# Optimization experiments

Hardware: AMD Instinct MI355X
Metric: run time of the kernel (lower is better)

## Reference

```python
import jax, jax.numpy as jnp
import numpy as np

WH, WW = 7, 7
N_HEADS = 6
INPUT_DIM = 192
HEAD_DIM = INPUT_DIM // N_HEADS
QK_SCALE = HEAD_DIM ** (-0.5)


def _relative_position_index(wh, ww):
    coords = np.stack(np.meshgrid(np.arange(wh), np.arange(ww), indexing='ij'))  # (2, wh, ww)
    cf = coords.reshape(2, -1)                       # (2, N)
    rel = cf[:, :, None] - cf[:, None, :]            # (2, N, N)
    rel = rel.transpose(1, 2, 0).copy()              # (N, N, 2)
    rel[:, :, 0] += wh - 1
    rel[:, :, 1] += ww - 1
    rel[:, :, 0] *= 2 * ww - 1
    return jnp.asarray(rel.sum(-1), dtype=jnp.int32)  # (N, N)

_REL_IDX = _relative_position_index(WH, WW)


def setup_inputs() -> dict:
    key = jax.random.key(0)
    ks = jax.random.split(key, 7)
    bW, nW = 4096, 64
    N = WH * WW
    s = 0.02
    return {
        "x": jax.random.normal(ks[0], (bW, WH, WW, INPUT_DIM), jnp.float32),
        "mask": jax.random.normal(ks[1], (nW, N, N), jnp.float32),
        "qkv_w": jax.random.normal(ks[2], (3 * INPUT_DIM, INPUT_DIM), jnp.float32) * s,
        "qkv_b": jax.random.normal(ks[3], (3 * INPUT_DIM,), jnp.float32) * s,
        "out_w": jax.random.normal(ks[4], (INPUT_DIM, INPUT_DIM), jnp.float32) * s,
        "out_b": jax.random.normal(ks[5], (INPUT_DIM,), jnp.float32) * s,
        "rpb_table": jax.random.normal(ks[6], ((2 * WH - 1) * (2 * WW - 1), N_HEADS), jnp.float32) * s,
    }


def reference(x, mask, qkv_w, qkv_b, out_w, out_b, rpb_table):
    b, Wh, Ww, C = x.shape
    N = Wh * Ww
    H, D = N_HEADS, HEAD_DIM
    # 1x1 conv == pointwise linear over channels-last input
    qkv = jnp.einsum('bxyc,oc->bxyo', x, qkv_w) + qkv_b          # (b, Wh, Ww, 3C)
    qkv = qkv.reshape(b, N, 3, H, D)                             # chunk order q,k,v; (h d) channel layout
    q, k, v = qkv[:, :, 0], qkv[:, :, 1], qkv[:, :, 2]           # (b, N, H, D)
    q = q * QK_SCALE
    sim = jnp.einsum('bihd,bjhd->bhij', q, k)                    # (b, H, N, N)
    # relative position bias gather
    rpb = rpb_table[_REL_IDX]                                    # (N, N, H)
    sim = sim + rpb.transpose(2, 0, 1)[None]                     # + (1, H, N, N)
    # shift mask add over windows
    nW = mask.shape[0]
    sim = sim.reshape(b // nW, nW, H, N, N) + mask[None, :, None]
    attn = jax.nn.softmax(sim, axis=-1).reshape(b, H, N, N)
    out = jnp.einsum('bhij,bjhd->bihd', attn, v)                 # (b, N, H, D)
    out = out.reshape(b, N, H * D)                               # (h d) channel order
    out = jnp.einsum('bnc,oc->bno', out, out_w) + out_b
    return out.reshape(b, Wh, Ww, C)
```

## Files before the change

### kernel.cpp

```cpp
#include <hip/hip_runtime.h>
#include <hip/hip_bf16.h>

typedef __bf16 bf16;
typedef __bf16 bf16x8 __attribute__((ext_vector_type(8)));
typedef float f32x4 __attribute__((ext_vector_type(4)));
typedef float floatv4 __attribute__((ext_vector_type(4)));

#define QK_SCALE 0.17677669529663687f

__device__ __forceinline__ bf16* qk_ptr(bf16* base, int row, int col) {
    return base + row * 32 + ((((col >> 3) ^ ((row >> 1) & 3)) << 3)) + (col & 7);
}
__device__ __forceinline__ bf16* vt_ptr(bf16* base, int row, int col) {
    return base + row * 64 + ((((col >> 3) ^ (row & 7)) << 3)) + (col & 7);
}
__device__ __forceinline__ bf16* ao_ptr(bf16* base, int row, int col) {
    return base + row * 192 + ((((col >> 3) ^ (row & 7)) << 3)) + (col & 7);
}

__global__ void wmsa_prep(const float* __restrict__ qkv_w,
                          const float* __restrict__ out_w,
                          const float* __restrict__ rpb_table,
                          const float* __restrict__ mask,
                          bf16* __restrict__ qkv_wb,
                          bf16* __restrict__ out_wb,
                          float* __restrict__ rpbx,
                          float* __restrict__ combo,
                          int build_combo) {
    int t = blockIdx.x * 256 + threadIdx.x;
    if (t < 110592) qkv_wb[t] = (bf16)qkv_w[t];
    if (t < 36864)  out_wb[t] = (bf16)out_w[t];
    if (t < 14406) {
        int h = t / 2401, ij = t % 2401, i = ij / 49, j = ij % 49;
        int ri = (i / 7 - j / 7 + 6) * 13 + (i % 7 - j % 7 + 6);
        rpbx[t] = rpb_table[ri * 6 + h];
    }
    if (build_combo && t < 64 * 6 * 64 * 64) {
        int j = t & 63, i = (t >> 6) & 63, r = t >> 12;
        int h = r % 6, w = r / 6;
        float v = -1e30f;
        if (i < 49 && j < 49) {
            int ri = (i / 7 - j / 7 + 6) * 13 + (i % 7 - j % 7 + 6);
            v = rpb_table[ri * 6 + h] + mask[w * 2401 + i * 49 + j];
        }
        combo[t] = v;
    }
}

template <bool USE_COMBO>
__global__ __launch_bounds__(768, 3) void wmsa_fused(
    const float* __restrict__ x, const float* __restrict__ mask,
    const float* __restrict__ qkv_b, const float* __restrict__ out_b,
    const bf16* __restrict__ qkv_wb, const bf16* __restrict__ out_wb,
    const float* __restrict__ rpbx, const float* __restrict__ combo,
    float* __restrict__ out)
{
    __shared__ __align__(16) bf16 s_x[12288];
    __shared__ __align__(16) bf16 s_qp[6][2048];
    __shared__ __align__(16) bf16 s_kao[12288];
    __shared__ __align__(16) bf16 s_vt[6][2048];

    const int b    = blockIdx.x;
    const int tid  = threadIdx.x;
    const int wv   = tid >> 6;
    const int lane = tid & 63;
    const int lo   = lane & 15;
    const int hi   = lane >> 4;

    const float* xw    = x + (size_t)b * 9408;
    const int    obase = wv * 48;
    const int    sec   = wv >> 2;

    {
        const int c0 = tid;
        const int r0s = c0 / 24, cc0 = c0 % 24;
        const float* p0 = xw + r0s * 192 + cc0 * 8;
        floatv4 f0 = *(const floatv4*)p0;
        floatv4 f1 = *(const floatv4*)(p0 + 4);
        bf16x8 v;
        v[0]=(bf16)f0[0]; v[1]=(bf16)f0[1]; v[2]=(bf16)f0[2]; v[3]=(bf16)f0[3];
        v[4]=(bf16)f1[0]; v[5]=(bf16)f1[1]; v[6]=(bf16)f1[2]; v[7]=(bf16)f1[3];
        *(bf16x8*)&s_x[(r0s * 24 + (cc0 ^ (r0s & 7))) * 8] = v;

        const int c1 = tid + 768;
        const int r1s = c1 / 24, cc1 = c1 % 24;
        bf16x8 w = {};
        if (r1s < 49) {
            const float* p1 = xw + r1s * 192 + cc1 * 8;
            floatv4 g0 = *(const floatv4*)p1;
            floatv4 g1 = *(const floatv4*)(p1 + 4);
            w[0]=(bf16)g0[0]; w[1]=(bf16)g0[1]; w[2]=(bf16)g0[2]; w[3]=(bf16)g0[3];
            w[4]=(bf16)g1[0]; w[5]=(bf16)g1[1]; w[6]=(bf16)g1[2]; w[7]=(bf16)g1[3];
        }
        *(bf16x8*)&s_x[(r1s * 24 + (cc1 ^ (r1s & 7))) * 8] = w;
    }
    __syncthreads();

#pragma unroll 1
    for (int mib = 0; mib < 2; ++mib) {
        f32x4 acc[2][3];
#pragma unroll
        for (int mi = 0; mi < 2; ++mi)
#pragma unroll
            for (int nj = 0; nj < 3; ++nj) acc[mi][nj] = (f32x4){0.f, 0.f, 0.f, 0.f};

        const int r0 = mib * 32 + lo;
        const int r1 = r0 + 16;

        auto loadB = [&](bf16x8* dst, int kk) {
#pragma unroll
            for (int nj = 0; nj < 3; ++nj)
                dst[nj] = *(const bf16x8*)(qkv_wb + (obase + nj * 16 + lo) * 192 + kk * 32 + hi * 8);
        };

        bf16x8 b0_[3], b1_[3], b2_[3];
        loadB(b0_, 0);
        loadB(b1_, 1);
#pragma unroll
        for (int kk = 0; kk < 6; ++kk) {
            if (kk < 4) loadB(b2_, kk + 2);
            bf16x8 a0 = *(const bf16x8*)ao_ptr(s_x, r0, kk * 32 + hi * 8);
            bf16x8 a1 = *(const bf16x8*)ao_ptr(s_x, r1, kk * 32 + hi * 8);
            acc[0][0] = __builtin_amdgcn_mfma_f32_16x16x32_bf16(a0, b0_[0], acc[0][0], 0, 0, 0);
            acc[1][0] = __builtin_amdgcn_mfma_f32_16x16x32_bf16(a1, b0_[0], acc[1][0], 0, 0, 0);
            acc[0][1] = __builtin_amdgcn_mfma_f32_16x16x32_bf16(a0, b0_[1], acc[0][1], 0, 0, 0);
            acc[1][1] = __builtin_amdgcn_mfma_f32_16x16x32_bf16(a1, b0_[1], acc[1][1], 0, 0, 0);
            acc[0][2] = __builtin_amdgcn_mfma_f32_16x16x32_bf16(a0, b0_[2], acc[0][2], 0, 0, 0);
            acc[1][2] = __builtin_amdgcn_mfma_f32_16x16x32_bf16(a1, b0_[2], acc[1][2], 0, 0, 0);
            b0_[0] = b1_[0]; b0_[1] = b1_[1]; b0_[2] = b1_[2];
            b1_[0] = b2_[0]; b1_[1] = b2_[1]; b1_[2] = b2_[2];
        }

#pragma unroll
        for (int nj = 0; nj < 3; ++nj) {
            const int o    = obase + nj * 16 + lo;
            const float bs = qkv_b[o];
            const int oc   = o - sec * 192;
            const int hh   = oc >> 5;
            const int dd   = oc & 31;
#pragma unroll
            for (int mi = 0; mi < 2; ++mi)
#pragma unroll
                for (int r = 0; r < 4; ++r) {
                    const int n = mib * 32 + mi * 16 + hi * 4 + r;
                    const float v = acc[mi][nj][r] + bs;
                    if (sec == 0)      *qk_ptr(&s_qp[hh][0], n, dd)      = (bf16)(v * QK_SCALE);
                    else if (sec == 1) *qk_ptr(s_kao + hh * 2048, n, dd) = (bf16)v;
                    else               *vt_ptr(&s_vt[hh][0], dd, n)      = (bf16)v;
                }
        }
    }
    __syncthreads();

    {
        const int h    = wv >> 1;
        const int p    = wv & 1;
        const int rowb = p * 32;
        bf16* qb    = &s_qp[h][0];
        bf16* kbase = s_kao + h * 2048;

        f32x4 cv[2][4];
        if (USE_COMBO) {
            const float* cb = combo + (((size_t)(b & 63) * 6 + h) << 12);
#pragma unroll
            for (int mi = 0; mi < 2; ++mi)
#pragma unroll
                for (int nt = 0; nt < 4; ++nt)
#pragma unroll
                    for (int r = 0; r < 4; ++r)
                        cv[mi][nt][r] = cb[(rowb + mi * 16 + hi * 4 + r) * 64 + nt * 16 + lo];
        }

        bf16x8 qa0 = *(const bf16x8*)qk_ptr(qb, rowb + lo, hi * 8);
        bf16x8 qa1 = *(const bf16x8*)qk_ptr(qb, rowb + 16 + lo, hi * 8);
        bf16x8 kb0 = *(const bf16x8*)qk_ptr(kbase,  0 + lo, hi * 8);
        bf16x8 kb1 = *(const bf16x8*)qk_ptr(kbase, 16 + lo, hi * 8);
        bf16x8 kb2 = *(const bf16x8*)qk_ptr(kbase, 32 + lo, hi * 8);
        bf16x8 kb3 = *(const bf16x8*)qk_ptr(kbase, 48 + lo, hi * 8);

        __syncthreads();

        f32x4 s[2][4];
#pragma unroll
        for (int mi = 0; mi < 2; ++mi)
#pragma unroll
            for (int nt = 0; nt < 4; ++nt) s[mi][nt] = (f32x4){0.f, 0.f, 0.f, 0.f};
        s[0][0] = __builtin_amdgcn_mfma_f32_16x16x32_bf16(qa0, kb0, s[0][0], 0, 0, 0);
        s[0][1] = __builtin_amdgcn_mfma_f32_16x16x32_bf16(qa0, kb1, s[0][1], 0, 0, 0);
        s[0][2] = __builtin_amdgcn_mfma_f32_16x16x32_bf16(qa0, kb2, s[0][2], 0, 0, 0);
        s[0][3] = __builtin_amdgcn_mfma_f32_16x16x32_bf16(qa0, kb3, s[0][3], 0, 0, 0);
        s[1][0] = __builtin_amdgcn_mfma_f32_16x16x32_bf16(qa1, kb0, s[1][0], 0, 0, 0);
        s[1][1] = __builtin_amdgcn_mfma_f32_16x16x32_bf16(qa1, kb1, s[1][1], 0, 0, 0);
        s[1][2] = __builtin_amdgcn_mfma_f32_16x16x32_bf16(qa1, kb2, s[1][2], 0, 0, 0);
        s[1][3] = __builtin_amdgcn_mfma_f32_16x16x32_bf16(qa1, kb3, s[1][3], 0, 0, 0);

        if (USE_COMBO) {
#pragma unroll
            for (int mi = 0; mi < 2; ++mi)
#pragma unroll
                for (int nt = 0; nt < 4; ++nt) s[mi][nt] += cv[mi][nt];
        } else {
            const float* mk = mask + (size_t)(b & 63) * 2401;
            const float* rb = rpbx + h * 2401;
#pragma unroll
            for (int nt = 0; nt < 4; ++nt) {
                const int j = nt * 16 + lo;
#pragma unroll
                for (int mi = 0; mi < 2; ++mi)
#pragma unroll
                    for (int r = 0; r < 4; ++r) {
                        const int i = rowb + mi * 16 + hi * 4 + r;
                        float sv = s[mi][nt][r];
                        if (j >= 49 || i >= 49) sv = -1e30f;
                        else sv += rb[i * 49 + j] + mk[i * 49 + j];
                        s[mi][nt][r] = sv;
                    }
            }
        }

#pragma unroll
        for (int mi = 0; mi < 2; ++mi)
#pragma unroll
            for (int r = 0; r < 4; ++r) {
                float m = fmaxf(fmaxf(s[mi][0][r], s[mi][1][r]),
                                fmaxf(s[mi][2][r], s[mi][3][r]));
                m = fmaxf(m, __shfl_xor(m, 1));
                m = fmaxf(m, __shfl_xor(m, 2));
                m = fmaxf(m, __shfl_xor(m, 4));
                m = fmaxf(m, __shfl_xor(m, 8));
                float sum = 0.f;
#pragma unroll
                for (int nt = 0; nt < 4; ++nt) {
                    float pv = __expf(s[mi][nt][r] - m);
                    s[mi][nt][r] = pv;
                    sum += pv;
                }
                sum += __shfl_xor(sum, 1);
                sum += __shfl_xor(sum, 2);
                sum += __shfl_xor(sum, 4);
                sum += __shfl_xor(sum, 8);
                const float inv = 1.0f / sum;
#pragma unroll
                for (int nt = 0; nt < 4; ++nt) s[mi][nt][r] *= inv;
            }

        f32x4 o00 = (f32x4){0.f,0.f,0.f,0.f}, o01 = (f32x4){0.f,0.f,0.f,0.f};
        f32x4 o10 = (f32x4){0.f,0.f,0.f,0.f}, o11 = (f32x4){0.f,0.f,0.f,0.f};
#pragma unroll
        for (int kk = 0; kk < 2; ++kk) {
#pragma unroll
            for (int mi = 0; mi < 2; ++mi)
#pragma unroll
                for (int c = 0; c < 2; ++c) {
                    const int nt = kk * 2 + c;
#pragma unroll
                    for (int r = 0; r < 4; ++r)
                        *qk_ptr(qb, rowb + mi * 16 + hi * 4 + r, c * 16 + lo) =
                            (bf16)s[mi][nt][r];
                }
            bf16x8 pa0 = *(const bf16x8*)qk_ptr(qb, rowb + lo, hi * 8);
            bf16x8 pa1 = *(const bf16x8*)qk_ptr(qb, rowb + 16 + lo, hi * 8);
            bf16x8 vb0 = *(const bf16x8*)vt_ptr(&s_vt[h][0],  0 + lo, kk * 32 + hi * 8);
            bf16x8 vb1 = *(const bf16x8*)vt_ptr(&s_vt[h][0], 16 + lo, kk * 32 + hi * 8);
            o00 = __builtin_amdgcn_mfma_f32_16x16x32_bf16(pa0, vb0, o00, 0, 0, 0);
            o10 = __builtin_amdgcn_mfma_f32_16x16x32_bf16(pa1, vb0, o10, 0, 0, 0);
            o01 = __builtin_amdgcn_mfma_f32_16x16x32_bf16(pa0, vb1, o01, 0, 0, 0);
            o11 = __builtin_amdgcn_mfma_f32_16x16x32_bf16(pa1, vb1, o11, 0, 0, 0);
        }

#pragma unroll
        for (int r = 0; r < 4; ++r) {
            const int n0 = rowb + hi * 4 + r;
            const int n1 = n0 + 16;
            *ao_ptr(s_kao, n0, h * 32 +  0 + lo) = (bf16)o00[r];
            *ao_ptr(s_kao, n0, h * 32 + 16 + lo) = (bf16)o01[r];
            *ao_ptr(s_kao, n1, h * 32 +  0 + lo) = (bf16)o10[r];
            *ao_ptr(s_kao, n1, h * 32 + 16 + lo) = (bf16)o11[r];
        }
    }
    __syncthreads();

    {
        const int o2 = wv * 16 + lo;
        f32x4 facc[4];
#pragma unroll
        for (int mi = 0; mi < 4; ++mi) facc[mi] = (f32x4){0.f, 0.f, 0.f, 0.f};

        bf16x8 fbc = *(const bf16x8*)(out_wb + o2 * 192 + hi * 8);
#pragma unroll
        for (int kk = 0; kk < 6; ++kk) {
            bf16x8 fbn;
            if (kk < 5) fbn = *(const bf16x8*)(out_wb + o2 * 192 + (kk + 1) * 32 + hi * 8);
            bf16x8 fa[4];
#pragma unroll
            for (int mi = 0; mi < 4; ++mi)
                fa[mi] = *(const bf16x8*)ao_ptr(s_kao, mi * 16 + lo, kk * 32 + hi * 8);
#pragma unroll
            for (int mi = 0; mi < 4; ++mi)
                facc[mi] = __builtin_amdgcn_mfma_f32_16x16x32_bf16(fa[mi], fbc, facc[mi], 0, 0, 0);
            fbc = fbn;
        }

        const float ob = out_b[o2];
        float* ow = out + (size_t)b * 9408;
#pragma unroll
        for (int mi = 0; mi < 4; ++mi)
#pragma unroll
            for (int r = 0; r < 4; ++r) {
                const int n = mi * 16 + hi * 4 + r;
                if (n < 49) ow[n * 192 + o2] = facc[mi][r] + ob;
            }
    }
}

extern "C" void kernel_launch(void* const* d_in, const int* in_sizes, int n_in,
                              void* d_out, int out_size, void* d_ws, size_t ws_size,
                              hipStream_t stream) {
    const float* x      = (const float*)d_in[0];
    const float* mask   = (const float*)d_in[1];
    const float* qkv_w  = (const float*)d_in[2];
    const float* qkv_b  = (const float*)d_in[3];
    const float* out_w  = (const float*)d_in[4];
    const float* out_b  = (const float*)d_in[5];
    const float* rpb    = (const float*)d_in[6];
    float* out          = (float*)d_out;

    char* ws = (char*)d_ws;
    bf16*  qkv_wb = (bf16*)ws;
    bf16*  out_wb = (bf16*)(ws + 221184);
    float* rpbx   = (float*)(ws + 294912);
    float* combo  = (float*)(ws + 352768);
    const bool use_combo = ws_size >= (size_t)(352768 + 6291456);

    hipLaunchKernelGGL(wmsa_prep, dim3(6144), dim3(256), 0, stream,
                       qkv_w, out_w, rpb, mask, qkv_wb, out_wb, rpbx, combo,
                       use_combo ? 1 : 0);
    if (use_combo)
        hipLaunchKernelGGL(HIP_KERNEL_NAME(wmsa_fused<true>), dim3(4096), dim3(768), 0, stream,
                           x, mask, qkv_b, out_b, qkv_wb, out_wb, rpbx, combo, out);
    else
        hipLaunchKernelGGL(HIP_KERNEL_NAME(wmsa_fused<false>), dim3(4096), dim3(768), 0, stream,
                           x, mask, qkv_b, out_b, qkv_wb, out_wb, rpbx, combo, out);
}
```

Measured before the change: 309.0 us.

## Transpose attention scores layout, vectorize LDS stores, prefetch combo bias and out weights

Computes S^T = K·Q^T so each lane holds a full query row's column slices, which reduces the softmax reductions to two cross-row shuffles. Q/K and V projections are written to LDS as packed 4-element bf16 stores using swapped MFMA operands. The combo bias table is stored transposed and loaded at kernel start, and all out-projection weights are loaded before the final barrier, so global latency overlaps earlier phases. The cost is higher register pressure at 768 threads with a minimum of 3 blocks per SM, which risks spills.

```diff
diff --git a/kernel.cpp b/kernel.cpp
--- a/kernel.cpp
+++ b/kernel.cpp
@@ -2,6 +2,7 @@
 #include <hip/hip_bf16.h>
 
 typedef __bf16 bf16;
+typedef __bf16 bf16x4 __attribute__((ext_vector_type(4)));
 typedef __bf16 bf16x8 __attribute__((ext_vector_type(8)));
 typedef float f32x4 __attribute__((ext_vector_type(4)));
 typedef float floatv4 __attribute__((ext_vector_type(4)));
@@ -25,7 +26,7 @@
                           bf16* __restrict__ qkv_wb,
                           bf16* __restrict__ out_wb,
                           float* __restrict__ rpbx,
-                          float* __restrict__ combo,
+                          float* __restrict__ comboT,
                           int build_combo) {
     int t = blockIdx.x * 256 + threadIdx.x;
     if (t < 110592) qkv_wb[t] = (bf16)qkv_w[t];
@@ -36,14 +37,14 @@
         rpbx[t] = rpb_table[ri * 6 + h];
     }
     if (build_combo && t < 64 * 6 * 64 * 64) {
-        int j = t & 63, i = (t >> 6) & 63, r = t >> 12;
+        int i = t & 63, j = (t >> 6) & 63, r = t >> 12;
         int h = r % 6, w = r / 6;
         float v = -1e30f;
         if (i < 49 && j < 49) {
             int ri = (i / 7 - j / 7 + 6) * 13 + (i % 7 - j % 7 + 6);
             v = rpb_table[ri * 6 + h] + mask[w * 2401 + i * 49 + j];
         }
-        combo[t] = v;
+        comboT[t] = v;
     }
 }
 
@@ -52,7 +53,7 @@
     const float* __restrict__ x, const float* __restrict__ mask,
     const float* __restrict__ qkv_b, const float* __restrict__ out_b,
     const bf16* __restrict__ qkv_wb, const bf16* __restrict__ out_wb,
-    const float* __restrict__ rpbx, const float* __restrict__ combo,
+    const float* __restrict__ rpbx, const float* __restrict__ comboT,
     float* __restrict__ out)
 {
     __shared__ __align__(16) bf16 s_x[12288];
@@ -70,6 +71,22 @@
     const float* xw    = x + (size_t)b * 9408;
     const int    obase = wv * 48;
     const int    sec   = wv >> 2;
+
+    const int ah   = wv >> 1;
+    const int arow = (wv & 1) * 32;
+
+    f32x4 cvT[2][4];
+    if (USE_COMBO) {
+        const float* cbT = comboT + (((size_t)(b & 63) * 6 + ah) << 12);
+#pragma unroll
+        for (int mq = 0; mq < 2; ++mq)
+#pragma unroll
+            for (int nt = 0; nt < 4; ++nt)
+#pragma unroll
+                for (int r = 0; r < 4; ++r)
+                    cvT[mq][nt][r] =
+                        cbT[(nt * 16 + hi * 4 + r) * 64 + arow + mq * 16 + lo];
+    }
 
     {
         const int c0 = tid;
@@ -121,163 +138,189 @@
             if (kk < 4) loadB(b2_, kk + 2);
             bf16x8 a0 = *(const bf16x8*)ao_ptr(s_x, r0, kk * 32 + hi * 8);
             bf16x8 a1 = *(const bf16x8*)ao_ptr(s_x, r1, kk * 32 + hi * 8);
-            acc[0][0] = __builtin_amdgcn_mfma_f32_16x16x32_bf16(a0, b0_[0], acc[0][0], 0, 0, 0);
-            acc[1][0] = __builtin_amdgcn_mfma_f32_16x16x32_bf16(a1, b0_[0], acc[1][0], 0, 0, 0);
-            acc[0][1] = __builtin_amdgcn_mfma_f32_16x16x32_bf16(a0, b0_[1], acc[0][1], 0, 0, 0);
-            acc[1][1] = __builtin_amdgcn_mfma_f32_16x16x32_bf16(a1, b0_[1], acc[1][1], 0, 0, 0);
-            acc[0][2] = __builtin_amdgcn_mfma_f32_16x16x32_bf16(a0, b0_[2], acc[0][2], 0, 0, 0);
-            acc[1][2] = __builtin_amdgcn_mfma_f32_16x16x32_bf16(a1, b0_[2], acc[1][2], 0, 0, 0);
+            if (sec < 2) {
+#pragma unroll
+                for (int nj = 0; nj < 3; ++nj) {
+                    acc[0][nj] = __builtin_amdgcn_mfma_f32_16x16x32_bf16(b0_[nj], a0, acc[0][nj], 0, 0, 0);
+                    acc[1][nj] = __builtin_amdgcn_mfma_f32_16x16x32_bf16(b0_[nj], a1, acc[1][nj], 0, 0, 0);
+                }
+            } else {
+#pragma unroll
+                for (int nj = 0; nj < 3; ++nj) {
+                    acc[0][nj] = __builtin_amdgcn_mfma_f32_16x16x32_bf16(a0, b0_[nj], acc[0][nj], 0, 0, 0);
+                    acc[1][nj] = __builtin_amdgcn_mfma_f32_16x16x32_bf16(a1, b0_[nj], acc[1][nj], 0, 0, 0);
+                }
+            }
             b0_[0] = b1_[0]; b0_[1] = b1_[1]; b0_[2] = b1_[2];
             b1_[0] = b2_[0]; b1_[1] = b2_[1]; b1_[2] = b2_[2];
         }
 
-#pragma unroll
-        for (int nj = 0; nj < 3; ++nj) {
-            const int o    = obase + nj * 16 + lo;
-            const float bs = qkv_b[o];
-            const int oc   = o - sec * 192;
-            const int hh   = oc >> 5;
-            const int dd   = oc & 31;
-#pragma unroll
-            for (int mi = 0; mi < 2; ++mi)
-#pragma unroll
-                for (int r = 0; r < 4; ++r) {
-                    const int n = mib * 32 + mi * 16 + hi * 4 + r;
-                    const float v = acc[mi][nj][r] + bs;
-                    if (sec == 0)      *qk_ptr(&s_qp[hh][0], n, dd)      = (bf16)(v * QK_SCALE);
-                    else if (sec == 1) *qk_ptr(s_kao + hh * 2048, n, dd) = (bf16)v;
-                    else               *vt_ptr(&s_vt[hh][0], dd, n)      = (bf16)v;
-                }
+        if (sec < 2) {
+#pragma unroll
+            for (int nj = 0; nj < 3; ++nj) {
+                const int ob4 = obase + nj * 16 + hi * 4;
+                floatv4 bs4 = *(const floatv4*)(qkv_b + ob4);
+                const int oc0 = ob4 - sec * 192;
+                const int hh  = oc0 >> 5;
+                const int dd  = oc0 & 31;
+                bf16* base = (sec == 0) ? &s_qp[hh][0] : (s_kao + hh * 2048);
+#pragma unroll
+                for (int mi = 0; mi < 2; ++mi) {
+                    const int n = mib * 32 + mi * 16 + lo;
+                    bf16x4 pk;
+#pragma unroll
+                    for (int r = 0; r < 4; ++r) {
+                        float v = acc[mi][nj][r] + bs4[r];
+                        if (sec == 0) v *= QK_SCALE;
+                        pk[r] = (bf16)v;
+                    }
+                    *(bf16x4*)qk_ptr(base, n, dd) = pk;
+                }
+            }
+        } else {
+#pragma unroll
+            for (int nj = 0; nj < 3; ++nj) {
+                const int o  = obase + nj * 16 + lo;
+                const float bs = qkv_b[o];
+                const int oc = o - 384;
+                const int hh = oc >> 5;
+                const int dd = oc & 31;
+#pragma unroll
+                for (int mi = 0; mi < 2; ++mi) {
+                    const int n0 = mib * 32 + mi * 16 + hi * 4;
+                    bf16x4 pk;
+#pragma unroll
+                    for (int r = 0; r < 4; ++r)
+                        pk[r] = (bf16)(acc[mi][nj][r] + bs);
+                    *(bf16x4*)vt_ptr(&s_vt[hh][0], dd, n0) = pk;
+                }
+            }
         }
     }
     __syncthreads();
 
+    f32x4 oacc[2][2];
+    bf16x8 fb[6];
     {
-        const int h    = wv >> 1;
-        const int p    = wv & 1;
-        const int rowb = p * 32;
-        bf16* qb    = &s_qp[h][0];
-        bf16* kbase = s_kao + h * 2048;
-
-        f32x4 cv[2][4];
+        bf16* qb    = &s_qp[ah][0];
+        bf16* kbase = s_kao + ah * 2048;
+
+        bf16x8 ka0 = *(const bf16x8*)qk_ptr(kbase,  0 + lo, hi * 8);
+        bf16x8 ka1 = *(const bf16x8*)qk_ptr(kbase, 16 + lo, hi * 8);
+        bf16x8 ka2 = *(const bf16x8*)qk_ptr(kbase, 32 + lo, hi * 8);
+        bf16x8 ka3 = *(const bf16x8*)qk_ptr(kbase, 48 + lo, hi * 8);
+        bf16x8 qb0 = *(const bf16x8*)qk_ptr(qb, arow + lo, hi * 8);
+        bf16x8 qb1 = *(const bf16x8*)qk_ptr(qb, arow + 16 + lo, hi * 8);
+
+        f32x4 t[4][2];
+#pragma unroll
+        for (int nt = 0; nt < 4; ++nt)
+#pragma unroll
+            for (int mq = 0; mq < 2; ++mq) t[nt][mq] = (f32x4){0.f, 0.f, 0.f, 0.f};
+        t[0][0] = __builtin_amdgcn_mfma_f32_16x16x32_bf16(ka0, qb0, t[0][0], 0, 0, 0);
+        t[1][0] = __builtin_amdgcn_mfma_f32_16x16x32_bf16(ka1, qb0, t[1][0], 0, 0, 0);
+        t[2][0] = __builtin_amdgcn_mfma_f32_16x16x32_bf16(ka2, qb0, t[2][0], 0, 0, 0);
+        t[3][0] = __builtin_amdgcn_mfma_f32_16x16x32_bf16(ka3, qb0, t[3][0], 0, 0, 0);
+        t[0][1] = __builtin_amdgcn_mfma_f32_16x16x32_bf16(ka0, qb1, t[0][1], 0, 0, 0);
+        t[1][1] = __builtin_amdgcn_mfma_f32_16x16x32_bf16(ka1, qb1, t[1][1], 0, 0, 0);
+        t[2][1] = __builtin_amdgcn_mfma_f32_16x16x32_bf16(ka2, qb1, t[2][1], 0, 0, 0);
+        t[3][1] = __builtin_amdgcn_mfma_f32_16x16x32_bf16(ka3, qb1, t[3][1], 0, 0, 0);
+
         if (USE_COMBO) {
-            const float* cb = combo + (((size_t)(b & 63) * 6 + h) << 12);
-#pragma unroll
-            for (int mi = 0; mi < 2; ++mi)
-#pragma unroll
-                for (int nt = 0; nt < 4; ++nt)
-#pragma unroll
-                    for (int r = 0; r < 4; ++r)
-                        cv[mi][nt][r] = cb[(rowb + mi * 16 + hi * 4 + r) * 64 + nt * 16 + lo];
-        }
-
-        bf16x8 qa0 = *(const bf16x8*)qk_ptr(qb, rowb + lo, hi * 8);
-        bf16x8 qa1 = *(const bf16x8*)qk_ptr(qb, rowb + 16 + lo, hi * 8);
-        bf16x8 kb0 = *(const bf16x8*)qk_ptr(kbase,  0 + lo, hi * 8);
-        bf16x8 kb1 = *(const bf16x8*)qk_ptr(kbase, 16 + lo, hi * 8);
-        bf16x8 kb2 = *(const bf16x8*)qk_ptr(kbase, 32 + lo, hi * 8);
-        bf16x8 kb3 = *(const bf16x8*)qk_ptr(kbase, 48 + lo, hi * 8);
-
-        __syncthreads();
-
-        f32x4 s[2][4];
-#pragma unroll
-        for (int mi = 0; mi < 2; ++mi)
-#pragma unroll
-            for (int nt = 0; nt < 4; ++nt) s[mi][nt] = (f32x4){0.f, 0.f, 0.f, 0.f};
-        s[0][0] = __builtin_amdgcn_mfma_f32_16x16x32_bf16(qa0, kb0, s[0][0], 0, 0, 0);
-        s[0][1] = __builtin_amdgcn_mfma_f32_16x16x32_bf16(qa0, kb1, s[0][1], 0, 0, 0);
-        s[0][2] = __builtin_amdgcn_mfma_f32_16x16x32_bf16(qa0, kb2, s[0][2], 0, 0, 0);
-        s[0][3] = __builtin_amdgcn_mfma_f32_16x16x32_bf16(qa0, kb3, s[0][3], 0, 0, 0);
-        s[1][0] = __builtin_amdgcn_mfma_f32_16x16x32_bf16(qa1, kb0, s[1][0], 0, 0, 0);
-        s[1][1] = __builtin_amdgcn_mfma_f32_16x16x32_bf16(qa1, kb1, s[1][1], 0, 0, 0);
-        s[1][2] = __builtin_amdgcn_mfma_f32_16x16x32_bf16(qa1, kb2, s[1][2], 0, 0, 0);
-        s[1][3] = __builtin_amdgcn_mfma_f32_16x16x32_bf16(qa1, kb3, s[1][3], 0, 0, 0);
-
-        if (USE_COMBO) {
-#pragma unroll
-            for (int mi = 0; mi < 2; ++mi)
-#pragma unroll
-                for (int nt = 0; nt < 4; ++nt) s[mi][nt] += cv[mi][nt];
+#pragma unroll
+            for (int nt = 0; nt < 4; ++nt)
+#pragma unroll
+                for (int mq = 0; mq < 2; ++mq) t[nt][mq] += cvT[mq][nt];
         } else {
             const float* mk = mask + (size_t)(b & 63) * 2401;
-            const float* rb = rpbx + h * 2401;
-#pragma unroll
-            for (int nt = 0; nt < 4; ++nt) {
-                const int j = nt * 16 + lo;
-#pragma unroll
-                for (int mi = 0; mi < 2; ++mi)
+            const float* rb = rpbx + ah * 2401;
+#pragma unroll
+            for (int nt = 0; nt < 4; ++nt)
+#pragma unroll
+                for (int mq = 0; mq < 2; ++mq)
 #pragma unroll
                     for (int r = 0; r < 4; ++r) {
-                        const int i = rowb + mi * 16 + hi * 4 + r;
-                        float sv = s[mi][nt][r];
+                        const int i = arow + mq * 16 + lo;
+                        const int j = nt * 16 + hi * 4 + r;
+                        float sv = t[nt][mq][r];
                         if (j >= 49 || i >= 49) sv = -1e30f;
                         else sv += rb[i * 49 + j] + mk[i * 49 + j];
-                        s[mi][nt][r] = sv;
+                        t[nt][mq][r] = sv;
                     }
-            }
-        }
-
-#pragma unroll
-        for (int mi = 0; mi < 2; ++mi)
-#pragma unroll
-            for (int r = 0; r < 4; ++r) {
-                float m = fmaxf(fmaxf(s[mi][0][r], s[mi][1][r]),
-                                fmaxf(s[mi][2][r], s[mi][3][r]));
-                m = fmaxf(m, __shfl_xor(m, 1));
-                m = fmaxf(m, __shfl_xor(m, 2));
-                m = fmaxf(m, __shfl_xor(m, 4));
-                m = fmaxf(m, __shfl_xor(m, 8));
-                float sum = 0.f;
-#pragma unroll
-                for (int nt = 0; nt < 4; ++nt) {
-                    float pv = __expf(s[mi][nt][r] - m);
-                    s[mi][nt][r] = pv;
-                    sum += pv;
-                }
-                sum += __shfl_xor(sum, 1);
-                sum += __shfl_xor(sum, 2);
-                sum += __shfl_xor(sum, 4);
-                sum += __shfl_xor(sum, 8);
-                const float inv = 1.0f / sum;
-#pragma unroll
-                for (int nt = 0; nt < 4; ++nt) s[mi][nt][r] *= inv;
-            }
-
-        f32x4 o00 = (f32x4){0.f,0.f,0.f,0.f}, o01 = (f32x4){0.f,0.f,0.f,0.f};
-        f32x4 o10 = (f32x4){0.f,0.f,0.f,0.f}, o11 = (f32x4){0.f,0.f,0.f,0.f};
+        }
+
+#pragma unroll
+        for (int mq = 0; mq < 2; ++mq) {
+            float m = fmaxf(fmaxf(t[0][mq][0], t[0][mq][1]),
+                            fmaxf(t[0][mq][2], t[0][mq][3]));
+#pragma unroll
+            for (int nt = 1; nt < 4; ++nt)
+                m = fmaxf(m, fmaxf(fmaxf(t[nt][mq][0], t[nt][mq][1]),
+                                   fmaxf(t[nt][mq][2], t[nt][mq][3])));
+            m = fmaxf(m, __shfl_xor(m, 16));
+            m = fmaxf(m, __shfl_xor(m, 32));
+            float sum = 0.f;
+#pragma unroll
+            for (int nt = 0; nt < 4; ++nt)
+#pragma unroll
+                for (int r = 0; r < 4; ++r) {
+                    float e = __expf(t[nt][mq][r] - m);
+                    t[nt][mq][r] = e;
+                    sum += e;
+                }
+            sum += __shfl_xor(sum, 16);
+            sum += __shfl_xor(sum, 32);
+            const float inv = 1.0f / sum;
+#pragma unroll
+            for (int nt = 0; nt < 4; ++nt)
+#pragma unroll
+                for (int r = 0; r < 4; ++r) t[nt][mq][r] *= inv;
+        }
+
+        {
+            const int o2 = wv * 16 + lo;
+#pragma unroll
+            for (int kk = 0; kk < 6; ++kk)
+                fb[kk] = *(const bf16x8*)(out_wb + o2 * 192 + kk * 32 + hi * 8);
+        }
+
+#pragma unroll
+        for (int mq = 0; mq < 2; ++mq)
+#pragma unroll
+            for (int nd = 0; nd < 2; ++nd) oacc[mq][nd] = (f32x4){0.f, 0.f, 0.f, 0.f};
+
 #pragma unroll
         for (int kk = 0; kk < 2; ++kk) {
 #pragma unroll
-            for (int mi = 0; mi < 2; ++mi)
+            for (int mq = 0; mq < 2; ++mq)
 #pragma unroll
                 for (int c = 0; c < 2; ++c) {
                     const int nt = kk * 2 + c;
-#pragma unroll
-                    for (int r = 0; r < 4; ++r)
-                        *qk_ptr(qb, rowb + mi * 16 + hi * 4 + r, c * 16 + lo) =
-                            (bf16)s[mi][nt][r];
-                }
-            bf16x8 pa0 = *(const bf16x8*)qk_ptr(qb, rowb + lo, hi * 8);
-            bf16x8 pa1 = *(const bf16x8*)qk_ptr(qb, rowb + 16 + lo, hi * 8);
-            bf16x8 vb0 = *(const bf16x8*)vt_ptr(&s_vt[h][0],  0 + lo, kk * 32 + hi * 8);
-            bf16x8 vb1 = *(const bf16x8*)vt_ptr(&s_vt[h][0], 16 + lo, kk * 32 + hi * 8);
-            o00 = __builtin_amdgcn_mfma_f32_16x16x32_bf16(pa0, vb0, o00, 0, 0, 0);
-            o10 = __builtin_amdgcn_mfma_f32_16x16x32_bf16(pa1, vb0, o10, 0, 0, 0);
-            o01 = __builtin_amdgcn_mfma_f32_16x16x32_bf16(pa0, vb1, o01, 0, 0, 0);
-            o11 = __builtin_amdgcn_mfma_f32_16x16x32_bf16(pa1, vb1, o11, 0, 0, 0);
-        }
-
-#pragma unroll
-        for (int r = 0; r < 4; ++r) {
-            const int n0 = rowb + hi * 4 + r;
-            const int n1 = n0 + 16;
-            *ao_ptr(s_kao, n0, h * 32 +  0 + lo) = (bf16)o00[r];
-            *ao_ptr(s_kao, n0, h * 32 + 16 + lo) = (bf16)o01[r];
-            *ao_ptr(s_kao, n1, h * 32 +  0 + lo) = (bf16)o10[r];
-            *ao_ptr(s_kao, n1, h * 32 + 16 + lo) = (bf16)o11[r];
-        }
-    }
+                    bf16x4 pk;
+#pragma unroll
+                    for (int r = 0; r < 4; ++r) pk[r] = (bf16)t[nt][mq][r];
+                    *(bf16x4*)qk_ptr(qb, arow + mq * 16 + lo, c * 16 + hi * 4) = pk;
+                }
+            bf16x8 pa0 = *(const bf16x8*)qk_ptr(qb, arow + lo, hi * 8);
+            bf16x8 pa1 = *(const bf16x8*)qk_ptr(qb, arow + 16 + lo, hi * 8);
+            bf16x8 vb0 = *(const bf16x8*)vt_ptr(&s_vt[ah][0],  0 + lo, kk * 32 + hi * 8);
+            bf16x8 vb1 = *(const bf16x8*)vt_ptr(&s_vt[ah][0], 16 + lo, kk * 32 + hi * 8);
+            oacc[0][0] = __builtin_amdgcn_mfma_f32_16x16x32_bf16(pa0, vb0, oacc[0][0], 0, 0, 0);
+            oacc[1][0] = __builtin_amdgcn_mfma_f32_16x16x32_bf16(pa1, vb0, oacc[1][0], 0, 0, 0);
+            oacc[0][1] = __builtin_amdgcn_mfma_f32_16x16x32_bf16(pa0, vb1, oacc[0][1], 0, 0, 0);
+            oacc[1][1] = __builtin_amdgcn_mfma_f32_16x16x32_bf16(pa1, vb1, oacc[1][1], 0, 0, 0);
+        }
+    }
+    __syncthreads();
+
+#pragma unroll
+    for (int mq = 0; mq < 2; ++mq)
+#pragma unroll
+        for (int nd = 0; nd < 2; ++nd)
+#pragma unroll
+            for (int r = 0; r < 4; ++r)
+                *ao_ptr(s_kao, arow + mq * 16 + hi * 4 + r,
+                        ah * 32 + nd * 16 + lo) = (bf16)oacc[mq][nd][r];
     __syncthreads();
 
     {
@@ -286,19 +329,15 @@
 #pragma unroll
         for (int mi = 0; mi < 4; ++mi) facc[mi] = (f32x4){0.f, 0.f, 0.f, 0.f};
 
-        bf16x8 fbc = *(const bf16x8*)(out_wb + o2 * 192 + hi * 8);
 #pragma unroll
         for (int kk = 0; kk < 6; ++kk) {
-            bf16x8 fbn;
-            if (kk < 5) fbn = *(const bf16x8*)(out_wb + o2 * 192 + (kk + 1) * 32 + hi * 8);
             bf16x8 fa[4];
 #pragma unroll
             for (int mi = 0; mi < 4; ++mi)
                 fa[mi] = *(const bf16x8*)ao_ptr(s_kao, mi * 16 + lo, kk * 32 + hi * 8);
 #pragma unroll
             for (int mi = 0; mi < 4; ++mi)
-                facc[mi] = __builtin_amdgcn_mfma_f32_16x16x32_bf16(fa[mi], fbc, facc[mi], 0, 0, 0);
-            fbc = fbn;
+                facc[mi] = __builtin_amdgcn_mfma_f32_16x16x32_bf16(fa[mi], fb[kk], facc[mi], 0, 0, 0);
         }
 
         const float ob = out_b[o2];
@@ -329,16 +368,16 @@
     bf16*  qkv_wb = (bf16*)ws;
     bf16*  out_wb = (bf16*)(ws + 221184);
     float* rpbx   = (float*)(ws + 294912);
-    float* combo  = (float*)(ws + 352768);
+    float* comboT = (float*)(ws + 352768);
     const bool use_combo = ws_size >= (size_t)(352768 + 6291456);
 
     hipLaunchKernelGGL(wmsa_prep, dim3(6144), dim3(256), 0, stream,
-                       qkv_w, out_w, rpb, mask, qkv_wb, out_wb, rpbx, combo,
+                       qkv_w, out_w, rpb, mask, qkv_wb, out_wb, rpbx, comboT,
                        use_combo ? 1 : 0);
     if (use_combo)
         hipLaunchKernelGGL(HIP_KERNEL_NAME(wmsa_fused<true>), dim3(4096), dim3(768), 0, stream,
-                           x, mask, qkv_b, out_b, qkv_wb, out_wb, rpbx, combo, out);
+                           x, mask, qkv_b, out_b, qkv_wb, out_wb, rpbx, comboT, out);
     else
         hipLaunchKernelGGL(HIP_KERNEL_NAME(wmsa_fused<false>), dim3(4096), dim3(768), 0, stream,
-                           x, mask, qkv_b, out_b, qkv_wb, out_wb, rpbx, combo, out);
-}
+                           x, mask, qkv_b, out_b, qkv_wb, out_wb, rpbx, comboT, out);
+}
```

Measured after the change: 356.6 us. 1.15x slower.

## Compact and alias shared memory buffers to fit two blocks per CU

Applied to the files above, without the earlier changes.

Replaces the four separate shared arrays with one packed buffer. It drops the padding rows beyond 49 tokens by clamping indices to a spare row, and aliases the attention-output tile onto the Q/K region. The aim is to cut LDS use enough that more than one 768-thread block can be resident per CU. It also folds log2(e) into the QK scale and the bias/mask so the softmax can use exp2, and moves a barrier to guard the aliased region. The trade-off is more index clamping and a tighter reliance on barrier placement for correctness.

```diff
diff --git a/kernel.cpp b/kernel.cpp
--- a/kernel.cpp
+++ b/kernel.cpp
@@ -6,7 +6,8 @@
 typedef float f32x4 __attribute__((ext_vector_type(4)));
 typedef float floatv4 __attribute__((ext_vector_type(4)));
 
-#define QK_SCALE 0.17677669529663687f
+#define LOG2E 1.4426950408889634f
+#define QK_SCALE2 (0.17677669529663687f * 1.4426950408889634f)
 
 __device__ __forceinline__ bf16* qk_ptr(bf16* base, int row, int col) {
     return base + row * 32 + ((((col >> 3) ^ ((row >> 1) & 3)) << 3)) + (col & 7);
@@ -14,7 +15,7 @@
 __device__ __forceinline__ bf16* vt_ptr(bf16* base, int row, int col) {
     return base + row * 64 + ((((col >> 3) ^ (row & 7)) << 3)) + (col & 7);
 }
-__device__ __forceinline__ bf16* ao_ptr(bf16* base, int row, int col) {
+__device__ __forceinline__ bf16* t192_ptr(bf16* base, int row, int col) {
     return base + row * 192 + ((((col >> 3) ^ (row & 7)) << 3)) + (col & 7);
 }
 
@@ -41,7 +42,7 @@
         float v = -1e30f;
         if (i < 49 && j < 49) {
             int ri = (i / 7 - j / 7 + 6) * 13 + (i % 7 - j % 7 + 6);
-            v = rpb_table[ri * 6 + h] + mask[w * 2401 + i * 49 + j];
+            v = (rpb_table[ri * 6 + h] + mask[w * 2401 + i * 49 + j]) * LOG2E;
         }
         combo[t] = v;
     }
@@ -55,10 +56,12 @@
     const float* __restrict__ rpbx, const float* __restrict__ combo,
     float* __restrict__ out)
 {
-    __shared__ __align__(16) bf16 s_x[12288];
-    __shared__ __align__(16) bf16 s_qp[6][2048];
-    __shared__ __align__(16) bf16 s_kao[12288];
-    __shared__ __align__(16) bf16 s_vt[6][2048];
+    __shared__ __align__(16) bf16 s_lds[40896];
+    bf16* s_x  = s_lds;
+    bf16* s_q  = s_lds + 9408;
+    bf16* s_k  = s_lds + 19008;
+    bf16* s_vt = s_lds + 28608;
+    bf16* s_ao = s_lds + 9408;
 
     const int b    = blockIdx.x;
     const int tid  = threadIdx.x;
@@ -71,28 +74,19 @@
     const int    obase = wv * 48;
     const int    sec   = wv >> 2;
 
-    {
-        const int c0 = tid;
-        const int r0s = c0 / 24, cc0 = c0 % 24;
-        const float* p0 = xw + r0s * 192 + cc0 * 8;
-        floatv4 f0 = *(const floatv4*)p0;
-        floatv4 f1 = *(const floatv4*)(p0 + 4);
-        bf16x8 v;
-        v[0]=(bf16)f0[0]; v[1]=(bf16)f0[1]; v[2]=(bf16)f0[2]; v[3]=(bf16)f0[3];
-        v[4]=(bf16)f1[0]; v[5]=(bf16)f1[1]; v[6]=(bf16)f1[2]; v[7]=(bf16)f1[3];
-        *(bf16x8*)&s_x[(r0s * 24 + (cc0 ^ (r0s & 7))) * 8] = v;
-
-        const int c1 = tid + 768;
-        const int r1s = c1 / 24, cc1 = c1 % 24;
-        bf16x8 w = {};
-        if (r1s < 49) {
-            const float* p1 = xw + r1s * 192 + cc1 * 8;
-            floatv4 g0 = *(const floatv4*)p1;
-            floatv4 g1 = *(const floatv4*)(p1 + 4);
-            w[0]=(bf16)g0[0]; w[1]=(bf16)g0[1]; w[2]=(bf16)g0[2]; w[3]=(bf16)g0[3];
-            w[4]=(bf16)g1[0]; w[5]=(bf16)g1[1]; w[6]=(bf16)g1[2]; w[7]=(bf16)g1[3];
-        }
-        *(bf16x8*)&s_x[(r1s * 24 + (cc1 ^ (r1s & 7))) * 8] = w;
+#pragma unroll
+    for (int q2 = 0; q2 < 2; ++q2) {
+        const int gc = q2 * 768 + tid;
+        if (gc < 1176) {
+            const int rs = gc / 24, cc = gc % 24;
+            const float* p = xw + rs * 192 + cc * 8;
+            floatv4 f0 = *(const floatv4*)p;
+            floatv4 f1 = *(const floatv4*)(p + 4);
+            bf16x8 v;
+            v[0]=(bf16)f0[0]; v[1]=(bf16)f0[1]; v[2]=(bf16)f0[2]; v[3]=(bf16)f0[3];
+            v[4]=(bf16)f1[0]; v[5]=(bf16)f1[1]; v[6]=(bf16)f1[2]; v[7]=(bf16)f1[3];
+            *(bf16x8*)&s_x[(rs * 24 + (cc ^ (rs & 7))) * 8] = v;
+        }
     }
     __syncthreads();
 
@@ -105,7 +99,7 @@
             for (int nj = 0; nj < 3; ++nj) acc[mi][nj] = (f32x4){0.f, 0.f, 0.f, 0.f};
 
         const int r0 = mib * 32 + lo;
-        const int r1 = r0 + 16;
+        const int r1 = min(r0 + 16, 48);
 
         auto loadB = [&](bf16x8* dst, int kk) {
 #pragma unroll
@@ -119,8 +113,8 @@
 #pragma unroll
         for (int kk = 0; kk < 6; ++kk) {
             if (kk < 4) loadB(b2_, kk + 2);
-            bf16x8 a0 = *(const bf16x8*)ao_ptr(s_x, r0, kk * 32 + hi * 8);
-            bf16x8 a1 = *(const bf16x8*)ao_ptr(s_x, r1, kk * 32 + hi * 8);
+            bf16x8 a0 = *(const bf16x8*)t192_ptr(s_x, r0, kk * 32 + hi * 8);
+            bf16x8 a1 = *(const bf16x8*)t192_ptr(s_x, r1, kk * 32 + hi * 8);
             acc[0][0] = __builtin_amdgcn_mfma_f32_16x16x32_bf16(a0, b0_[0], acc[0][0], 0, 0, 0);
             acc[1][0] = __builtin_amdgcn_mfma_f32_16x16x32_bf16(a1, b0_[0], acc[1][0], 0, 0, 0);
             acc[0][1] = __builtin_amdgcn_mfma_f32_16x16x32_bf16(a0, b0_[1], acc[0][1], 0, 0, 0);
@@ -142,11 +136,12 @@
             for (int mi = 0; mi < 2; ++mi)
 #pragma unroll
                 for (int r = 0; r < 4; ++r) {
-                    const int n = mib * 32 + mi * 16 + hi * 4 + r;
+                    const int n  = mib * 32 + mi * 16 + hi * 4 + r;
+                    const int nc = min(n, 49);
                     const float v = acc[mi][nj][r] + bs;
-                    if (sec == 0)      *qk_ptr(&s_qp[hh][0], n, dd)      = (bf16)(v * QK_SCALE);
-                    else if (sec == 1) *qk_ptr(s_kao + hh * 2048, n, dd) = (bf16)v;
-                    else               *vt_ptr(&s_vt[hh][0], dd, n)      = (bf16)v;
+                    if (sec == 0)      *qk_ptr(s_q + hh * 1600, nc, dd) = (bf16)(v * QK_SCALE2);
+                    else if (sec == 1) *qk_ptr(s_k + hh * 1600, nc, dd) = (bf16)v;
+                    else               *vt_ptr(s_vt + hh * 2048, dd, n) = (bf16)v;
                 }
         }
     }
@@ -154,10 +149,9 @@
 
     {
         const int h    = wv >> 1;
-        const int p    = wv & 1;
-        const int rowb = p * 32;
-        bf16* qb    = &s_qp[h][0];
-        bf16* kbase = s_kao + h * 2048;
+        const int rowb = (wv & 1) * 32;
+        bf16* qb    = s_q + h * 1600;
+        bf16* kbase = s_k + h * 1600;
 
         f32x4 cv[2][4];
         if (USE_COMBO) {
@@ -172,13 +166,11 @@
         }
 
         bf16x8 qa0 = *(const bf16x8*)qk_ptr(qb, rowb + lo, hi * 8);
-        bf16x8 qa1 = *(const bf16x8*)qk_ptr(qb, rowb + 16 + lo, hi * 8);
+        bf16x8 qa1 = *(const bf16x8*)qk_ptr(qb, min(rowb + 16 + lo, 49), hi * 8);
         bf16x8 kb0 = *(const bf16x8*)qk_ptr(kbase,  0 + lo, hi * 8);
         bf16x8 kb1 = *(const bf16x8*)qk_ptr(kbase, 16 + lo, hi * 8);
         bf16x8 kb2 = *(const bf16x8*)qk_ptr(kbase, 32 + lo, hi * 8);
-        bf16x8 kb3 = *(const bf16x8*)qk_ptr(kbase, 48 + lo, hi * 8);
-
-        __syncthreads();
+        bf16x8 kb3 = *(const bf16x8*)qk_ptr(kbase, min(48 + lo, 49), hi * 8);
 
         f32x4 s[2][4];
 #pragma unroll
@@ -212,7 +204,7 @@
                         const int i = rowb + mi * 16 + hi * 4 + r;
                         float sv = s[mi][nt][r];
                         if (j >= 49 || i >= 49) sv = -1e30f;
-                        else sv += rb[i * 49 + j] + mk[i * 49 + j];
+                        else sv += (rb[i * 49 + j] + mk[i * 49 + j]) * LOG2E;
                         s[mi][nt][r] = sv;
                     }
             }
@@ -231,7 +223,7 @@
                 float sum = 0.f;
 #pragma unroll
                 for (int nt = 0; nt < 4; ++nt) {
-                    float pv = __expf(s[mi][nt][r] - m);
+                    float pv = exp2f(s[mi][nt][r] - m);
                     s[mi][nt][r] = pv;
                     sum += pv;
                 }
@@ -255,27 +247,28 @@
                     const int nt = kk * 2 + c;
 #pragma unroll
                     for (int r = 0; r < 4; ++r)
-                        *qk_ptr(qb, rowb + mi * 16 + hi * 4 + r, c * 16 + lo) =
+                        *qk_ptr(qb, min(rowb + mi * 16 + hi * 4 + r, 49), c * 16 + lo) =
                             (bf16)s[mi][nt][r];
                 }
             bf16x8 pa0 = *(const bf16x8*)qk_ptr(qb, rowb + lo, hi * 8);
-            bf16x8 pa1 = *(const bf16x8*)qk_ptr(qb, rowb + 16 + lo, hi * 8);
-            bf16x8 vb0 = *(const bf16x8*)vt_ptr(&s_vt[h][0],  0 + lo, kk * 32 + hi * 8);
-            bf16x8 vb1 = *(const bf16x8*)vt_ptr(&s_vt[h][0], 16 + lo, kk * 32 + hi * 8);
+            bf16x8 pa1 = *(const bf16x8*)qk_ptr(qb, min(rowb + 16 + lo, 49), hi * 8);
+            bf16x8 vb0 = *(const bf16x8*)vt_ptr(s_vt + h * 2048,  0 + lo, kk * 32 + hi * 8);
+            bf16x8 vb1 = *(const bf16x8*)vt_ptr(s_vt + h * 2048, 16 + lo, kk * 32 + hi * 8);
             o00 = __builtin_amdgcn_mfma_f32_16x16x32_bf16(pa0, vb0, o00, 0, 0, 0);
             o10 = __builtin_amdgcn_mfma_f32_16x16x32_bf16(pa1, vb0, o10, 0, 0, 0);
             o01 = __builtin_amdgcn_mfma_f32_16x16x32_bf16(pa0, vb1, o01, 0, 0, 0);
             o11 = __builtin_amdgcn_mfma_f32_16x16x32_bf16(pa1, vb1, o11, 0, 0, 0);
         }
+        __syncthreads();
 
 #pragma unroll
         for (int r = 0; r < 4; ++r) {
             const int n0 = rowb + hi * 4 + r;
             const int n1 = n0 + 16;
-            *ao_ptr(s_kao, n0, h * 32 +  0 + lo) = (bf16)o00[r];
-            *ao_ptr(s_kao, n0, h * 32 + 16 + lo) = (bf16)o01[r];
-            *ao_ptr(s_kao, n1, h * 32 +  0 + lo) = (bf16)o10[r];
-            *ao_ptr(s_kao, n1, h * 32 + 16 + lo) = (bf16)o11[r];
+            *t192_ptr(s_ao, n0, (wv >> 1) * 32 +  0 + lo) = (bf16)o00[r];
+            *t192_ptr(s_ao, n0, (wv >> 1) * 32 + 16 + lo) = (bf16)o01[r];
+            *t192_ptr(s_ao, n1, (wv >> 1) * 32 +  0 + lo) = (bf16)o10[r];
+            *t192_ptr(s_ao, n1, (wv >> 1) * 32 + 16 + lo) = (bf16)o11[r];
         }
     }
     __syncthreads();
@@ -294,7 +287,7 @@
             bf16x8 fa[4];
 #pragma unroll
             for (int mi = 0; mi < 4; ++mi)
-                fa[mi] = *(const bf16x8*)ao_ptr(s_kao, mi * 16 + lo, kk * 32 + hi * 8);
+                fa[mi] = *(const bf16x8*)t192_ptr(s_ao, mi * 16 + lo, kk * 32 + hi * 8);
 #pragma unroll
             for (int mi = 0; mi < 4; ++mi)
                 facc[mi] = __builtin_amdgcn_mfma_f32_16x16x32_bf16(fa[mi], fbc, facc[mi], 0, 0, 0);
```

New measurement: 323.0 us. +4.5%, slower.
